# Optimization experiments

Hardware: AMD Instinct MI355X
Metric: run time of the kernel (lower is better)

Reference implementation:

```python
import jax, jax.numpy as jnp
import numpy as np

N = 50000
E = 800000
IN = 256
HID = 64
H12 = 4
LAT = 32
NEG_SLOPE = 0.2


def gat_conv(x, src, dst, W, a_src, a_dst, b, heads, out_ch, concat):
    """PyG GATConv (eval mode, add_self_loops already applied to src/dst).
    x: [N, F_in]; src/dst: [Etot]; W: [F_in, heads*out_ch]; a_*: [heads, out_ch]; b: bias.
    Returns (out, alpha[Etot, heads])."""
    n = x.shape[0]
    h = (x @ W).reshape(n, heads, out_ch)                 # [N,H,C]
    e_src = (h * a_src).sum(-1)                           # [N,H]
    e_dst = (h * a_dst).sum(-1)                           # [N,H]
    e = jax.nn.leaky_relu(e_src[src] + e_dst[dst], NEG_SLOPE)   # [Etot,H]
    emax = jax.ops.segment_max(e, dst, num_segments=n)
    ee = jnp.exp(e - emax[dst])
    denom = jax.ops.segment_sum(ee, dst, num_segments=n)
    alpha = ee / (denom[dst] + 1e-16)                     # segment softmax over incoming edges
    msg = h[src] * alpha[:, :, None]                      # [Etot,H,C]
    out = jax.ops.segment_sum(msg, dst, num_segments=n)   # [N,H,C]
    out = out.reshape(n, heads * out_ch) if concat else out.mean(axis=1)
    return out + b, alpha


def setup_inputs() -> dict:
    key = jax.random.key(0)
    ks = jax.random.split(key, 20)
    s = 0.1
    inp = {
        "x": jax.random.normal(ks[0], (N, IN), jnp.float32),
        "edge_index": jax.random.randint(ks[1], (2, E), 0, N, jnp.int32),
        "W1": jax.random.normal(ks[2], (IN, H12 * HID), jnp.float32) * s,
        "a1s": jax.random.normal(ks[3], (H12, HID), jnp.float32) * s,
        "a1d": jax.random.normal(ks[4], (H12, HID), jnp.float32) * s,
        "b1": jnp.zeros((H12 * HID,), jnp.float32),
        "W2": jax.random.normal(ks[5], (H12 * HID, H12 * HID), jnp.float32) * s,
        "a2s": jax.random.normal(ks[6], (H12, HID), jnp.float32) * s,
        "a2d": jax.random.normal(ks[7], (H12, HID), jnp.float32) * s,
        "b2": jnp.zeros((HID,), jnp.float32),
        "Wm": jax.random.normal(ks[8], (HID, LAT), jnp.float32) * s,
        "ams": jax.random.normal(ks[9], (1, LAT), jnp.float32) * s,
        "amd": jax.random.normal(ks[10], (1, LAT), jnp.float32) * s,
        "bm": jnp.zeros((LAT,), jnp.float32),
        # log_std head
        "Ws": jax.random.normal(ks[11], (HID, LAT), jnp.float32) * s,
        "ass": jax.random.normal(ks[12], (1, LAT), jnp.float32) * s,
        "asd": jax.random.normal(ks[13], (1, LAT), jnp.float32) * s,
        "bs": jnp.zeros((LAT,), jnp.float32),
    }
    return inp


def reference(x, edge_index, W1, a1s, a1d, b1, W2, a2s, a2d, b2,
              Wm, ams, amd, bm, Ws, ass, asd, bs):
    # GATConv adds self loops by default
    loops = jnp.arange(N, dtype=edge_index.dtype)
    src = jnp.concatenate([edge_index[0], loops])
    dst = jnp.concatenate([edge_index[1], loops])

    h1, a_w1 = gat_conv(x, src, dst, W1, a1s, a1d, b1, H12, HID, True)
    h1 = jax.nn.relu(h1)
    h2, a_w2 = gat_conv(h1, src, dst, W2, a2s, a2d, b2, H12, HID, False)
    h2 = jax.nn.relu(h2)  # dropout is identity in eval mode
    z_mean, a_wm = gat_conv(h2, src, dst, Wm, ams, amd, bm, 1, LAT, False)
    z_log_std, a_ws = gat_conv(h2, src, dst, Ws, ass, asd, bs, 1, LAT, False)
    return (z_mean, z_log_std, a_w1, a_w2, a_wm, a_ws)
```

## Files before the change

### kernel.cpp

```cpp
#include <hip/hip_runtime.h>
#include <cstdint>
#include <cstddef>

#define NN 50000
#define EE 800000
#define ETOT 850000
#define NEG_SLOPE 0.2f

typedef _Float16 f16;
typedef __attribute__((ext_vector_type(4))) _Float16 f16x4;
typedef __attribute__((ext_vector_type(8))) _Float16 f16x8;
typedef __attribute__((ext_vector_type(4))) float f32x4;


__global__ __launch_bounds__(256) void deg_kernel(const int* __restrict__ ei, int* __restrict__ deg) {
    int e = blockIdx.x * 256 + threadIdx.x;
    if (e >= ETOT) return;
    int d = (e < EE) ? ei[EE + e] : (e - EE);
    atomicAdd(&deg[d], 1);
}

__global__ __launch_bounds__(256) void scan1_kernel(const int* __restrict__ deg, int* __restrict__ offs,
                                                    int* __restrict__ bsum, int n) {
    __shared__ int sh[256];
    int i = blockIdx.x * 256 + threadIdx.x;
    int v = (i < n) ? deg[i] : 0;
    sh[threadIdx.x] = v;
    __syncthreads();
    for (int off = 1; off < 256; off <<= 1) {
        int t = (threadIdx.x >= off) ? sh[threadIdx.x - off] : 0;
        __syncthreads();
        sh[threadIdx.x] += t;
        __syncthreads();
    }
    if (i < n) offs[i] = sh[threadIdx.x] - v;
    if (threadIdx.x == 255) bsum[blockIdx.x] = sh[255];
}

__global__ __launch_bounds__(256) void scan2_kernel(int* __restrict__ bsum, int nb) {
    __shared__ int sh[256];
    int v = (threadIdx.x < nb) ? bsum[threadIdx.x] : 0;
    sh[threadIdx.x] = v;
    __syncthreads();
    for (int off = 1; off < 256; off <<= 1) {
        int t = (threadIdx.x >= off) ? sh[threadIdx.x - off] : 0;
        __syncthreads();
        sh[threadIdx.x] += t;
        __syncthreads();
    }
    if (threadIdx.x < nb) bsum[threadIdx.x] = sh[threadIdx.x] - v;
}

__global__ __launch_bounds__(256) void scan3_kernel(const int* __restrict__ bsum, int* __restrict__ offs,
                                                    int* __restrict__ cursor, int n) {
    int i = blockIdx.x * 256 + threadIdx.x;
    if (i < n) {
        int o = offs[i] + bsum[blockIdx.x];
        offs[i] = o;
        cursor[i] = o;
    }
}

__global__ __launch_bounds__(256) void fill_kernel(const int* __restrict__ ei, int* __restrict__ cursor,
                                                   int* __restrict__ csrc, int* __restrict__ ceid) {
    int e = blockIdx.x * 256 + threadIdx.x;
    if (e >= ETOT) return;
    int d, s;
    if (e < EE) { s = ei[e]; d = ei[EE + e]; } else { s = e - EE; d = e - EE; }
    int p = atomicAdd(&cursor[d], 1);
    csrc[p] = s;
    ceid[p] = e;
}


template<int K, bool AF32>
__global__ __launch_bounds__(256) void mfma_gemm(const void* __restrict__ Ap, const f16* __restrict__ Bt,
                                                 f16* __restrict__ C, int M, int N) {
    int w = threadIdx.x >> 6, lane = threadIdx.x & 63;
    int m0 = blockIdx.y * 128 + w * 32;
    int n0 = blockIdx.x * 64;
    int r = lane & 15, kb = lane >> 4;
    int ar0 = m0 + r;       if (ar0 > M - 1) ar0 = M - 1;
    int ar1 = m0 + 16 + r;  if (ar1 > M - 1) ar1 = M - 1;
    f32x4 acc[2][4] = {};
    const float* Af = (const float*)Ap;
    const f16*   Ah = (const f16*)Ap;
    size_t a0off = (size_t)ar0 * K + kb * 8;
    size_t a1off = (size_t)ar1 * K + kb * 8;
    const f16* bbase = Bt + (size_t)(n0 + r) * K + kb * 8;
    for (int k0 = 0; k0 < K; k0 += 32) {
        f16x8 a0, a1;
        if constexpr (AF32) {
            float4 l0 = *(const float4*)(Af + a0off + k0);
            float4 h0 = *(const float4*)(Af + a0off + k0 + 4);
            float4 l1 = *(const float4*)(Af + a1off + k0);
            float4 h1 = *(const float4*)(Af + a1off + k0 + 4);
            a0[0]=(f16)l0.x; a0[1]=(f16)l0.y; a0[2]=(f16)l0.z; a0[3]=(f16)l0.w;
            a0[4]=(f16)h0.x; a0[5]=(f16)h0.y; a0[6]=(f16)h0.z; a0[7]=(f16)h0.w;
            a1[0]=(f16)l1.x; a1[1]=(f16)l1.y; a1[2]=(f16)l1.z; a1[3]=(f16)l1.w;
            a1[4]=(f16)h1.x; a1[5]=(f16)h1.y; a1[6]=(f16)h1.z; a1[7]=(f16)h1.w;
        } else {
            a0 = *(const f16x8*)(Ah + a0off + k0);
            a1 = *(const f16x8*)(Ah + a1off + k0);
        }
#pragma unroll
        for (int ni = 0; ni < 4; ++ni) {
            f16x8 b = *(const f16x8*)(bbase + (size_t)ni * 16 * K + k0);
            acc[0][ni] = __builtin_amdgcn_mfma_f32_16x16x32_f16(a0, b, acc[0][ni], 0, 0, 0);
            acc[1][ni] = __builtin_amdgcn_mfma_f32_16x16x32_f16(a1, b, acc[1][ni], 0, 0, 0);
        }
    }
#pragma unroll
    for (int mi = 0; mi < 2; ++mi) {
#pragma unroll
        for (int i = 0; i < 4; ++i) {
            int row = m0 + mi * 16 + kb * 4 + i;
            if (row < M) {
#pragma unroll
                for (int ni = 0; ni < 4; ++ni)
                    C[(size_t)row * N + n0 + ni * 16 + r] = (f16)acc[mi][ni][i];
            }
        }
    }
}


__global__ __launch_bounds__(256) void packw_kernel(const float* __restrict__ W1, const float* __restrict__ W2,
                                                    const float* __restrict__ Wm, const float* __restrict__ Ws,
                                                    const float* __restrict__ ams, const float* __restrict__ ass,
                                                    const float* __restrict__ amd, const float* __restrict__ asd,
                                                    f16* __restrict__ Wt1, f16* __restrict__ Wt2,
                                                    f16* __restrict__ Wtms,
                                                    float* __restrict__ aS, float* __restrict__ aD) {
    int i = blockIdx.x * 256 + threadIdx.x;
    if (i < 65536) {
        int n = i >> 8, k = i & 255;
        Wt1[(size_t)n * 256 + k] = (f16)W1[(size_t)k * 256 + n];
        Wt2[(size_t)n * 256 + k] = (f16)W2[(size_t)k * 256 + n];
    }
    if (i < 4096) {
        int c = i >> 6, k = i & 63;
        float v = (c < 32) ? Wm[k * 32 + c] : Ws[k * 32 + (c - 32)];
        Wtms[(size_t)c * 64 + k] = (f16)v;
    }
    if (i < 64) {
        aS[i] = (i < 32) ? ams[i] : ass[i - 32];
        aD[i] = (i < 32) ? amd[i] : asd[i - 32];
    }
}


__global__ __launch_bounds__(256) void scores4_kernel(const f16* __restrict__ H, const float* __restrict__ aS,
                                                      const float* __restrict__ aD, float* __restrict__ es,
                                                      float* __restrict__ ed) {
    int wave = threadIdx.x >> 6, lane = threadIdx.x & 63;
    int n = blockIdx.x * 4 + wave;
    if (n >= NN) return;
    f16x4 h = *(const f16x4*)(H + (size_t)n * 256 + lane * 4);
    float4 s4 = *(const float4*)(aS + lane * 4);
    float4 d4 = *(const float4*)(aD + lane * 4);
    float hx = (float)h[0], hy = (float)h[1], hz = (float)h[2], hw = (float)h[3];
    float ps = hx * s4.x + hy * s4.y + hz * s4.z + hw * s4.w;
    float pd = hx * d4.x + hy * d4.y + hz * d4.z + hw * d4.w;
    for (int off = 1; off < 16; off <<= 1) { ps += __shfl_xor(ps, off); pd += __shfl_xor(pd, off); }
    if ((lane & 15) == 0) {
        int hh = lane >> 4;
        es[n * 4 + hh] = ps;
        ed[n * 4 + hh] = pd;
    }
}

__global__ __launch_bounds__(256) void scores_ms_kernel(const f16* __restrict__ H, const float* __restrict__ aS,
                                                        const float* __restrict__ aD, float* __restrict__ es,
                                                        float* __restrict__ ed) {
    int wave = threadIdx.x >> 6, lane = threadIdx.x & 63;
    int n = blockIdx.x * 4 + wave;
    if (n >= NN) return;
    float h = (float)H[(size_t)n * 64 + lane];
    float ps = h * aS[lane];
    float pd = h * aD[lane];
    for (int off = 1; off < 32; off <<= 1) { ps += __shfl_xor(ps, off); pd += __shfl_xor(pd, off); }
    if ((lane & 31) == 0) {
        int g = lane >> 5;
        es[n * 2 + g] = ps;
        ed[n * 2 + g] = pd;
    }
}

__device__ __forceinline__ float leaky(float v) { return v > 0.f ? v : NEG_SLOPE * v; }


__global__ __launch_bounds__(256) void agg_concat_kernel(
    const f16* __restrict__ H, const float* __restrict__ es, const float* __restrict__ ed,
    const int* __restrict__ offs, const int* __restrict__ csrc, const int* __restrict__ ceid,
    const float* __restrict__ bias, f16* __restrict__ out, float* __restrict__ alpha_out) {
    int wave = threadIdx.x >> 6, lane = threadIdx.x & 63;
    int n = blockIdx.x * 4 + wave;
    if (n >= NN) return;
    int start = offs[n];
    int end = (n + 1 < NN) ? offs[n + 1] : ETOT;
    int deg = end - start;
    int h16 = lane >> 4, sub = lane & 15;
    float edh = ed[n * 4 + h16];
    float dsum = 0.f;
    for (int j = sub; j < deg; j += 16) {
        int s = csrc[start + j];
        dsum += __expf(leaky(es[s * 4 + h16] + edh));
    }
    for (int off = 1; off < 16; off <<= 1) dsum += __shfl_xor(dsum, off);
    float inv = 1.f / (dsum + 1e-16f);
    int half = lane >> 5;
    int l5 = lane & 31;
    int hh = l5 >> 3;
    int c8 = l5 * 8;
    float invh = __shfl(inv, hh << 4);
    float edhh = __shfl(edh, hh << 4);
    bool writer = ((l5 & 7) == 0);
    float accv[8] = {};
    int j = half;
    for (; j + 6 < deg; j += 8) {
        int p0 = start + j, p1 = start + j + 2, p2 = start + j + 4, p3 = start + j + 6;
        int s0 = csrc[p0], s1 = csrc[p1], s2 = csrc[p2], s3 = csrc[p3];
        float a0 = __expf(leaky(es[s0 * 4 + hh] + edhh)) * invh;
        float a1 = __expf(leaky(es[s1 * 4 + hh] + edhh)) * invh;
        float a2 = __expf(leaky(es[s2 * 4 + hh] + edhh)) * invh;
        float a3 = __expf(leaky(es[s3 * 4 + hh] + edhh)) * invh;
        if (writer) {
            alpha_out[(size_t)ceid[p0] * 4 + hh] = a0;
            alpha_out[(size_t)ceid[p1] * 4 + hh] = a1;
            alpha_out[(size_t)ceid[p2] * 4 + hh] = a2;
            alpha_out[(size_t)ceid[p3] * 4 + hh] = a3;
        }
        f16x8 v0 = *(const f16x8*)(H + (size_t)s0 * 256 + c8);
        f16x8 v1 = *(const f16x8*)(H + (size_t)s1 * 256 + c8);
        f16x8 v2 = *(const f16x8*)(H + (size_t)s2 * 256 + c8);
        f16x8 v3 = *(const f16x8*)(H + (size_t)s3 * 256 + c8);
#pragma unroll
        for (int k = 0; k < 8; ++k)
            accv[k] += a0 * (float)v0[k] + a1 * (float)v1[k] + a2 * (float)v2[k] + a3 * (float)v3[k];
    }
    for (; j < deg; j += 2) {
        int p0 = start + j;
        int s0 = csrc[p0];
        float a0 = __expf(leaky(es[s0 * 4 + hh] + edhh)) * invh;
        if (writer) alpha_out[(size_t)ceid[p0] * 4 + hh] = a0;
        f16x8 v0 = *(const f16x8*)(H + (size_t)s0 * 256 + c8);
#pragma unroll
        for (int k = 0; k < 8; ++k) accv[k] += a0 * (float)v0[k];
    }
#pragma unroll
    for (int k = 0; k < 8; ++k) accv[k] += __shfl_xor(accv[k], 32);
    if (lane < 32) {
        f16x8 r;
#pragma unroll
        for (int k = 0; k < 8; ++k) r[k] = (f16)fmaxf(accv[k] + bias[c8 + k], 0.f);
        *(f16x8*)(out + (size_t)n * 256 + c8) = r;
    }
}


__global__ __launch_bounds__(256) void agg_mean_kernel(
    const f16* __restrict__ H, const float* __restrict__ es, const float* __restrict__ ed,
    const int* __restrict__ offs, const int* __restrict__ csrc, const int* __restrict__ ceid,
    const float* __restrict__ bias, f16* __restrict__ out, float* __restrict__ alpha_out) {
    int wave = threadIdx.x >> 6, lane = threadIdx.x & 63;
    int n = blockIdx.x * 4 + wave;
    if (n >= NN) return;
    int start = offs[n];
    int end = (n + 1 < NN) ? offs[n + 1] : ETOT;
    int deg = end - start;
    int h16 = lane >> 4, sub = lane & 15;
    float edh = ed[n * 4 + h16];
    float dsum = 0.f;
    for (int j = sub; j < deg; j += 16) {
        int s = csrc[start + j];
        dsum += __expf(leaky(es[s * 4 + h16] + edh));
    }
    for (int off = 1; off < 16; off <<= 1) dsum += __shfl_xor(dsum, off);
    float inv = 1.f / (dsum + 1e-16f);
    int half = lane >> 5;
    int l5 = lane & 31;
    int hh = l5 >> 3;
    int c8 = l5 * 8;
    float invh = __shfl(inv, hh << 4);
    float edhh = __shfl(edh, hh << 4);
    bool writer = ((l5 & 7) == 0);
    float accv[8] = {};
    int j = half;
    for (; j + 6 < deg; j += 8) {
        int p0 = start + j, p1 = start + j + 2, p2 = start + j + 4, p3 = start + j + 6;
        int s0 = csrc[p0], s1 = csrc[p1], s2 = csrc[p2], s3 = csrc[p3];
        float a0 = __expf(leaky(es[s0 * 4 + hh] + edhh)) * invh;
        float a1 = __expf(leaky(es[s1 * 4 + hh] + edhh)) * invh;
        float a2 = __expf(leaky(es[s2 * 4 + hh] + edhh)) * invh;
        float a3 = __expf(leaky(es[s3 * 4 + hh] + edhh)) * invh;
        if (writer) {
            alpha_out[(size_t)ceid[p0] * 4 + hh] = a0;
            alpha_out[(size_t)ceid[p1] * 4 + hh] = a1;
            alpha_out[(size_t)ceid[p2] * 4 + hh] = a2;
            alpha_out[(size_t)ceid[p3] * 4 + hh] = a3;
        }
        f16x8 v0 = *(const f16x8*)(H + (size_t)s0 * 256 + c8);
        f16x8 v1 = *(const f16x8*)(H + (size_t)s1 * 256 + c8);
        f16x8 v2 = *(const f16x8*)(H + (size_t)s2 * 256 + c8);
        f16x8 v3 = *(const f16x8*)(H + (size_t)s3 * 256 + c8);
#pragma unroll
        for (int k = 0; k < 8; ++k)
            accv[k] += a0 * (float)v0[k] + a1 * (float)v1[k] + a2 * (float)v2[k] + a3 * (float)v3[k];
    }
    for (; j < deg; j += 2) {
        int p0 = start + j;
        int s0 = csrc[p0];
        float a0 = __expf(leaky(es[s0 * 4 + hh] + edhh)) * invh;
        if (writer) alpha_out[(size_t)ceid[p0] * 4 + hh] = a0;
        f16x8 v0 = *(const f16x8*)(H + (size_t)s0 * 256 + c8);
#pragma unroll
        for (int k = 0; k < 8; ++k) accv[k] += a0 * (float)v0[k];
    }
#pragma unroll
    for (int k = 0; k < 8; ++k) {
        accv[k] += __shfl_xor(accv[k], 8);
        accv[k] += __shfl_xor(accv[k], 16);
        accv[k] += __shfl_xor(accv[k], 32);
    }
    if (lane < 8) {
        f16x8 r;
#pragma unroll
        for (int k = 0; k < 8; ++k) r[k] = (f16)fmaxf(accv[k] * 0.25f + bias[lane * 8 + k], 0.f);
        *(f16x8*)(out + (size_t)n * 64 + lane * 8) = r;
    }
}


__global__ __launch_bounds__(256) void agg_ms_kernel(
    const f16* __restrict__ H, const float* __restrict__ es, const float* __restrict__ ed,
    const int* __restrict__ offs, const int* __restrict__ csrc, const int* __restrict__ ceid,
    const float* __restrict__ bm, const float* __restrict__ bs,
    float* __restrict__ zmean, float* __restrict__ zlog,
    float* __restrict__ a_wm, float* __restrict__ a_ws) {
    int wave = threadIdx.x >> 6, lane = threadIdx.x & 63;
    int n = blockIdx.x * 4 + wave;
    if (n >= NN) return;
    int start = offs[n];
    int end = (n + 1 < NN) ? offs[n + 1] : ETOT;
    int deg = end - start;
    int g = lane >> 5, sub = lane & 31;
    float edg = ed[n * 2 + g];
    float dsum = 0.f;
    for (int j = sub; j < deg; j += 32) {
        int s = csrc[start + j];
        dsum += __expf(leaky(es[s * 2 + g] + edg));
    }
    for (int off = 1; off < 32; off <<= 1) dsum += __shfl_xor(dsum, off);
    float inv = 1.f / (dsum + 1e-16f);
    int slot = lane >> 3;
    int le = lane & 7;
    int g2 = le >> 2;
    int c8 = le * 8;
    float invg = __shfl(inv, g2 << 5);
    float edg2 = __shfl(edg, g2 << 5);
    float accv[8] = {};
    for (int j = slot; j < deg; j += 8) {
        int p = start + j;
        int s = csrc[p];
        float a = __expf(leaky(es[s * 2 + g2] + edg2)) * invg;
        if (le == 0) a_wm[ceid[p]] = a;
        else if (le == 4) a_ws[ceid[p]] = a;
        f16x8 v = *(const f16x8*)(H + (size_t)s * 64 + c8);
#pragma unroll
        for (int k = 0; k < 8; ++k) accv[k] += a * (float)v[k];
    }
#pragma unroll
    for (int k = 0; k < 8; ++k) {
        accv[k] += __shfl_xor(accv[k], 8);
        accv[k] += __shfl_xor(accv[k], 16);
        accv[k] += __shfl_xor(accv[k], 32);
    }
    if (lane < 4) {
        float4 r0, r1;
        int cb = lane * 8;
        r0.x = accv[0] + bm[cb + 0]; r0.y = accv[1] + bm[cb + 1];
        r0.z = accv[2] + bm[cb + 2]; r0.w = accv[3] + bm[cb + 3];
        r1.x = accv[4] + bm[cb + 4]; r1.y = accv[5] + bm[cb + 5];
        r1.z = accv[6] + bm[cb + 6]; r1.w = accv[7] + bm[cb + 7];
        *(float4*)(zmean + (size_t)n * 32 + cb) = r0;
        *(float4*)(zmean + (size_t)n * 32 + cb + 4) = r1;
    } else if (lane < 8) {
        float4 r0, r1;
        int cb = (lane - 4) * 8;
        r0.x = accv[0] + bs[cb + 0]; r0.y = accv[1] + bs[cb + 1];
        r0.z = accv[2] + bs[cb + 2]; r0.w = accv[3] + bs[cb + 3];
        r1.x = accv[4] + bs[cb + 4]; r1.y = accv[5] + bs[cb + 5];
        r1.z = accv[6] + bs[cb + 6]; r1.w = accv[7] + bs[cb + 7];
        *(float4*)(zlog + (size_t)n * 32 + cb) = r0;
        *(float4*)(zlog + (size_t)n * 32 + cb + 4) = r1;
    }
}


extern "C" void kernel_launch(void* const* d_in, const int* in_sizes, int n_in,
                              void* d_out, int out_size, void* d_ws, size_t ws_size,
                              hipStream_t stream) {
    const float* x   = (const float*)d_in[0];
    const int*   ei  = (const int*)d_in[1];
    const float* W1  = (const float*)d_in[2];
    const float* a1s = (const float*)d_in[3];
    const float* a1d = (const float*)d_in[4];
    const float* b1  = (const float*)d_in[5];
    const float* W2  = (const float*)d_in[6];
    const float* a2s = (const float*)d_in[7];
    const float* a2d = (const float*)d_in[8];
    const float* b2  = (const float*)d_in[9];
    const float* Wm  = (const float*)d_in[10];
    const float* ams = (const float*)d_in[11];
    const float* amd = (const float*)d_in[12];
    const float* bm  = (const float*)d_in[13];
    const float* Ws  = (const float*)d_in[14];
    const float* ass = (const float*)d_in[15];
    const float* asd = (const float*)d_in[16];
    const float* bs  = (const float*)d_in[17];

    float* out = (float*)d_out;
    float* zmean = out;
    float* zlog  = out + 1600000;
    float* a_w1  = out + 3200000;
    float* a_w2  = out + 6600000;
    float* a_wm  = out + 10000000;
    float* a_ws_o = out + 10850000;

    float* ws = (float*)d_ws;
    size_t o = 0;
    f16*   Hh   = (f16*)(ws + o); o += (size_t)NN * 128;
    f16*   h1h  = (f16*)(ws + o); o += (size_t)NN * 128;
    f16*   h2h  = (f16*)(ws + o); o += (size_t)NN * 32;
    float* es1  = ws + o; o += NN * 4;
    float* ed1  = ws + o; o += NN * 4;
    float* es2  = ws + o; o += NN * 4;
    float* ed2  = ws + o; o += NN * 4;
    float* esms = ws + o; o += NN * 2;
    float* edms = ws + o; o += NN * 2;
    f16*   Wt1  = (f16*)(ws + o); o += 32768;
    f16*   Wt2  = (f16*)(ws + o); o += 32768;
    f16*   Wtms = (f16*)(ws + o); o += 2048;
    float* aSms = ws + o; o += 64;
    float* aDms = ws + o; o += 64;
    int* deg    = (int*)(ws + o); o += NN;
    int* offs   = (int*)(ws + o); o += NN;
    int* cursor = (int*)(ws + o); o += NN;
    int* csrc   = (int*)(ws + o); o += ETOT;
    int* ceid   = (int*)(ws + o); o += ETOT;

    const int edgeBlocks = (ETOT + 255) / 256;
    const int nodeBlocks = (NN + 255) / 256;
    const int waveBlocks = (NN + 3) / 4;

    hipMemsetAsync(deg, 0, NN * sizeof(int), stream);
    deg_kernel<<<edgeBlocks, 256, 0, stream>>>(ei, deg);
    scan1_kernel<<<nodeBlocks, 256, 0, stream>>>(deg, offs, cursor , NN);
    scan2_kernel<<<1, 256, 0, stream>>>(cursor, nodeBlocks);
    scan3_kernel<<<nodeBlocks, 256, 0, stream>>>(cursor, offs, deg , NN);
    fill_kernel<<<edgeBlocks, 256, 0, stream>>>(ei, deg, csrc, ceid);

    packw_kernel<<<256, 256, 0, stream>>>(W1, W2, Wm, Ws, ams, ass, amd, asd, Wt1, Wt2, Wtms, aSms, aDms);

    dim3 gg1(4, (NN + 127) / 128);
    dim3 gg3(1, (NN + 127) / 128);
    mfma_gemm<256, true><<<gg1, 256, 0, stream>>>(x, Wt1, Hh, NN, 256);
    scores4_kernel<<<waveBlocks, 256, 0, stream>>>(Hh, a1s, a1d, es1, ed1);
    agg_concat_kernel<<<waveBlocks, 256, 0, stream>>>(Hh, es1, ed1, offs, csrc, ceid, b1, h1h, a_w1);

    mfma_gemm<256, false><<<gg1, 256, 0, stream>>>(h1h, Wt2, Hh, NN, 256);
    scores4_kernel<<<waveBlocks, 256, 0, stream>>>(Hh, a2s, a2d, es2, ed2);
    agg_mean_kernel<<<waveBlocks, 256, 0, stream>>>(Hh, es2, ed2, offs, csrc, ceid, b2, h2h, a_w2);

    mfma_gemm<64, false><<<gg3, 256, 0, stream>>>(h2h, Wtms, Hh, NN, 64);
    scores_ms_kernel<<<waveBlocks, 256, 0, stream>>>(Hh, aSms, aDms, esms, edms);
    agg_ms_kernel<<<waveBlocks, 256, 0, stream>>>(Hh, esms, edms, offs, csrc, ceid, bm, bs,
                                                  zmean, zlog, a_wm, a_ws_o);
}
```

Before: 546.6 us.

## Move attention-weight output to coalesced per-edge kernels and drop edge-id permutation

The aggregation kernels no longer scatter alpha values through the CSR edge-id array. Instead they store the per-node softmax inverse denominators, and new edge-parallel kernels recompute alpha in original edge order with coalesced vector stores. This removes the ceid array along with its fill-time writes and gather reads, at the cost of extra launches that re-read edge_index, the scores and the inverses. Aggregation blocks also shrink from four waves to two.

```diff
diff --git a/kernel.cpp b/kernel.cpp
--- a/kernel.cpp
+++ b/kernel.cpp
@@ -62,14 +62,13 @@
 }
 
 __global__ __launch_bounds__(256) void fill_kernel(const int* __restrict__ ei, int* __restrict__ cursor,
-                                                   int* __restrict__ csrc, int* __restrict__ ceid) {
+                                                   int* __restrict__ csrc) {
     int e = blockIdx.x * 256 + threadIdx.x;
     if (e >= ETOT) return;
     int d, s;
     if (e < EE) { s = ei[e]; d = ei[EE + e]; } else { s = e - EE; d = e - EE; }
     int p = atomicAdd(&cursor[d], 1);
     csrc[p] = s;
-    ceid[p] = e;
 }
 
 
@@ -190,12 +189,45 @@
 __device__ __forceinline__ float leaky(float v) { return v > 0.f ? v : NEG_SLOPE * v; }
 
 
-__global__ __launch_bounds__(256) void agg_concat_kernel(
+__global__ __launch_bounds__(256) void alpha4_kernel(const int* __restrict__ ei, const float* __restrict__ es,
+                                                     const float* __restrict__ ed, const float* __restrict__ inv,
+                                                     float* __restrict__ out4) {
+    int e = blockIdx.x * 256 + threadIdx.x;
+    if (e >= ETOT) return;
+    int s, d;
+    if (e < EE) { s = ei[e]; d = ei[EE + e]; } else { s = e - EE; d = e - EE; }
+    float4 esv = *(const float4*)(es + (size_t)s * 4);
+    float4 edv = *(const float4*)(ed + (size_t)d * 4);
+    float4 iv  = *(const float4*)(inv + (size_t)d * 4);
+    float4 r;
+    r.x = __expf(leaky(esv.x + edv.x)) * iv.x;
+    r.y = __expf(leaky(esv.y + edv.y)) * iv.y;
+    r.z = __expf(leaky(esv.z + edv.z)) * iv.z;
+    r.w = __expf(leaky(esv.w + edv.w)) * iv.w;
+    *(float4*)(out4 + (size_t)e * 4) = r;
+}
+
+__global__ __launch_bounds__(256) void alpha_ms_kernel(const int* __restrict__ ei, const float* __restrict__ es,
+                                                       const float* __restrict__ ed, const float* __restrict__ inv,
+                                                       float* __restrict__ awm, float* __restrict__ aws) {
+    int e = blockIdx.x * 256 + threadIdx.x;
+    if (e >= ETOT) return;
+    int s, d;
+    if (e < EE) { s = ei[e]; d = ei[EE + e]; } else { s = e - EE; d = e - EE; }
+    float2 esv = *(const float2*)(es + (size_t)s * 2);
+    float2 edv = *(const float2*)(ed + (size_t)d * 2);
+    float2 iv  = *(const float2*)(inv + (size_t)d * 2);
+    awm[e] = __expf(leaky(esv.x + edv.x)) * iv.x;
+    aws[e] = __expf(leaky(esv.y + edv.y)) * iv.y;
+}
+
+
+__global__ __launch_bounds__(128) void agg_concat_kernel(
     const f16* __restrict__ H, const float* __restrict__ es, const float* __restrict__ ed,
-    const int* __restrict__ offs, const int* __restrict__ csrc, const int* __restrict__ ceid,
-    const float* __restrict__ bias, f16* __restrict__ out, float* __restrict__ alpha_out) {
+    const int* __restrict__ offs, const int* __restrict__ csrc,
+    const float* __restrict__ bias, f16* __restrict__ out, float* __restrict__ invout) {
     int wave = threadIdx.x >> 6, lane = threadIdx.x & 63;
-    int n = blockIdx.x * 4 + wave;
+    int n = blockIdx.x * 2 + wave;
     if (n >= NN) return;
     int start = offs[n];
     int end = (n + 1 < NN) ? offs[n + 1] : ETOT;
@@ -209,13 +241,13 @@
     }
     for (int off = 1; off < 16; off <<= 1) dsum += __shfl_xor(dsum, off);
     float inv = 1.f / (dsum + 1e-16f);
+    if (sub == 0) invout[n * 4 + h16] = inv;
     int half = lane >> 5;
     int l5 = lane & 31;
     int hh = l5 >> 3;
     int c8 = l5 * 8;
     float invh = __shfl(inv, hh << 4);
     float edhh = __shfl(edh, hh << 4);
-    bool writer = ((l5 & 7) == 0);
     float accv[8] = {};
     int j = half;
     for (; j + 6 < deg; j += 8) {
@@ -225,12 +257,6 @@
         float a1 = __expf(leaky(es[s1 * 4 + hh] + edhh)) * invh;
         float a2 = __expf(leaky(es[s2 * 4 + hh] + edhh)) * invh;
         float a3 = __expf(leaky(es[s3 * 4 + hh] + edhh)) * invh;
-        if (writer) {
-            alpha_out[(size_t)ceid[p0] * 4 + hh] = a0;
-            alpha_out[(size_t)ceid[p1] * 4 + hh] = a1;
-            alpha_out[(size_t)ceid[p2] * 4 + hh] = a2;
-            alpha_out[(size_t)ceid[p3] * 4 + hh] = a3;
-        }
         f16x8 v0 = *(const f16x8*)(H + (size_t)s0 * 256 + c8);
         f16x8 v1 = *(const f16x8*)(H + (size_t)s1 * 256 + c8);
         f16x8 v2 = *(const f16x8*)(H + (size_t)s2 * 256 + c8);
@@ -243,7 +269,6 @@
         int p0 = start + j;
         int s0 = csrc[p0];
         float a0 = __expf(leaky(es[s0 * 4 + hh] + edhh)) * invh;
-        if (writer) alpha_out[(size_t)ceid[p0] * 4 + hh] = a0;
         f16x8 v0 = *(const f16x8*)(H + (size_t)s0 * 256 + c8);
 #pragma unroll
         for (int k = 0; k < 8; ++k) accv[k] += a0 * (float)v0[k];
@@ -259,12 +284,12 @@
 }
 
 
-__global__ __launch_bounds__(256) void agg_mean_kernel(
+__global__ __launch_bounds__(128) void agg_mean_kernel(
     const f16* __restrict__ H, const float* __restrict__ es, const float* __restrict__ ed,
-    const int* __restrict__ offs, const int* __restrict__ csrc, const int* __restrict__ ceid,
-    const float* __restrict__ bias, f16* __restrict__ out, float* __restrict__ alpha_out) {
+    const int* __restrict__ offs, const int* __restrict__ csrc,
+    const float* __restrict__ bias, f16* __restrict__ out, float* __restrict__ invout) {
     int wave = threadIdx.x >> 6, lane = threadIdx.x & 63;
-    int n = blockIdx.x * 4 + wave;
+    int n = blockIdx.x * 2 + wave;
     if (n >= NN) return;
     int start = offs[n];
     int end = (n + 1 < NN) ? offs[n + 1] : ETOT;
@@ -278,13 +303,13 @@
     }
     for (int off = 1; off < 16; off <<= 1) dsum += __shfl_xor(dsum, off);
     float inv = 1.f / (dsum + 1e-16f);
+    if (sub == 0) invout[n * 4 + h16] = inv;
     int half = lane >> 5;
     int l5 = lane & 31;
     int hh = l5 >> 3;
     int c8 = l5 * 8;
     float invh = __shfl(inv, hh << 4);
     float edhh = __shfl(edh, hh << 4);
-    bool writer = ((l5 & 7) == 0);
     float accv[8] = {};
     int j = half;
     for (; j + 6 < deg; j += 8) {
@@ -294,12 +319,6 @@
         float a1 = __expf(leaky(es[s1 * 4 + hh] + edhh)) * invh;
         float a2 = __expf(leaky(es[s2 * 4 + hh] + edhh)) * invh;
         float a3 = __expf(leaky(es[s3 * 4 + hh] + edhh)) * invh;
-        if (writer) {
-            alpha_out[(size_t)ceid[p0] * 4 + hh] = a0;
-            alpha_out[(size_t)ceid[p1] * 4 + hh] = a1;
-            alpha_out[(size_t)ceid[p2] * 4 + hh] = a2;
-            alpha_out[(size_t)ceid[p3] * 4 + hh] = a3;
-        }
         f16x8 v0 = *(const f16x8*)(H + (size_t)s0 * 256 + c8);
         f16x8 v1 = *(const f16x8*)(H + (size_t)s1 * 256 + c8);
         f16x8 v2 = *(const f16x8*)(H + (size_t)s2 * 256 + c8);
@@ -312,7 +331,6 @@
         int p0 = start + j;
         int s0 = csrc[p0];
         float a0 = __expf(leaky(es[s0 * 4 + hh] + edhh)) * invh;
-        if (writer) alpha_out[(size_t)ceid[p0] * 4 + hh] = a0;
         f16x8 v0 = *(const f16x8*)(H + (size_t)s0 * 256 + c8);
 #pragma unroll
         for (int k = 0; k < 8; ++k) accv[k] += a0 * (float)v0[k];
@@ -332,14 +350,13 @@
 }
 
 
-__global__ __launch_bounds__(256) void agg_ms_kernel(
+__global__ __launch_bounds__(128) void agg_ms_kernel(
     const f16* __restrict__ H, const float* __restrict__ es, const float* __restrict__ ed,
-    const int* __restrict__ offs, const int* __restrict__ csrc, const int* __restrict__ ceid,
+    const int* __restrict__ offs, const int* __restrict__ csrc,
     const float* __restrict__ bm, const float* __restrict__ bs,
-    float* __restrict__ zmean, float* __restrict__ zlog,
-    float* __restrict__ a_wm, float* __restrict__ a_ws) {
+    float* __restrict__ zmean, float* __restrict__ zlog, float* __restrict__ invout) {
     int wave = threadIdx.x >> 6, lane = threadIdx.x & 63;
-    int n = blockIdx.x * 4 + wave;
+    int n = blockIdx.x * 2 + wave;
     if (n >= NN) return;
     int start = offs[n];
     int end = (n + 1 < NN) ? offs[n + 1] : ETOT;
@@ -353,6 +370,7 @@
     }
     for (int off = 1; off < 32; off <<= 1) dsum += __shfl_xor(dsum, off);
     float inv = 1.f / (dsum + 1e-16f);
+    if (sub == 0) invout[n * 2 + g] = inv;
     int slot = lane >> 3;
     int le = lane & 7;
     int g2 = le >> 2;
@@ -364,8 +382,6 @@
         int p = start + j;
         int s = csrc[p];
         float a = __expf(leaky(es[s * 2 + g2] + edg2)) * invg;
-        if (le == 0) a_wm[ceid[p]] = a;
-        else if (le == 4) a_ws[ceid[p]] = a;
         f16x8 v = *(const f16x8*)(H + (size_t)s * 64 + c8);
 #pragma unroll
         for (int k = 0; k < 8; ++k) accv[k] += a * (float)v[k];
@@ -439,6 +455,9 @@
     float* ed2  = ws + o; o += NN * 4;
     float* esms = ws + o; o += NN * 2;
     float* edms = ws + o; o += NN * 2;
+    float* inv1 = ws + o; o += NN * 4;
+    float* inv2 = ws + o; o += NN * 4;
+    float* invms= ws + o; o += NN * 2;
     f16*   Wt1  = (f16*)(ws + o); o += 32768;
     f16*   Wt2  = (f16*)(ws + o); o += 32768;
     f16*   Wtms = (f16*)(ws + o); o += 2048;
@@ -448,18 +467,18 @@
     int* offs   = (int*)(ws + o); o += NN;
     int* cursor = (int*)(ws + o); o += NN;
     int* csrc   = (int*)(ws + o); o += ETOT;
-    int* ceid   = (int*)(ws + o); o += ETOT;
 
     const int edgeBlocks = (ETOT + 255) / 256;
     const int nodeBlocks = (NN + 255) / 256;
     const int waveBlocks = (NN + 3) / 4;
+    const int aggBlocks  = (NN + 1) / 2;
 
     hipMemsetAsync(deg, 0, NN * sizeof(int), stream);
     deg_kernel<<<edgeBlocks, 256, 0, stream>>>(ei, deg);
     scan1_kernel<<<nodeBlocks, 256, 0, stream>>>(deg, offs, cursor , NN);
     scan2_kernel<<<1, 256, 0, stream>>>(cursor, nodeBlocks);
     scan3_kernel<<<nodeBlocks, 256, 0, stream>>>(cursor, offs, deg , NN);
-    fill_kernel<<<edgeBlocks, 256, 0, stream>>>(ei, deg, csrc, ceid);
+    fill_kernel<<<edgeBlocks, 256, 0, stream>>>(ei, deg, csrc);
 
     packw_kernel<<<256, 256, 0, stream>>>(W1, W2, Wm, Ws, ams, ass, amd, asd, Wt1, Wt2, Wtms, aSms, aDms);
 
@@ -467,14 +486,17 @@
     dim3 gg3(1, (NN + 127) / 128);
     mfma_gemm<256, true><<<gg1, 256, 0, stream>>>(x, Wt1, Hh, NN, 256);
     scores4_kernel<<<waveBlocks, 256, 0, stream>>>(Hh, a1s, a1d, es1, ed1);
-    agg_concat_kernel<<<waveBlocks, 256, 0, stream>>>(Hh, es1, ed1, offs, csrc, ceid, b1, h1h, a_w1);
+    agg_concat_kernel<<<aggBlocks, 128, 0, stream>>>(Hh, es1, ed1, offs, csrc, b1, h1h, inv1);
+    alpha4_kernel<<<edgeBlocks, 256, 0, stream>>>(ei, es1, ed1, inv1, a_w1);
 
     mfma_gemm<256, false><<<gg1, 256, 0, stream>>>(h1h, Wt2, Hh, NN, 256);
     scores4_kernel<<<waveBlocks, 256, 0, stream>>>(Hh, a2s, a2d, es2, ed2);
-    agg_mean_kernel<<<waveBlocks, 256, 0, stream>>>(Hh, es2, ed2, offs, csrc, ceid, b2, h2h, a_w2);
+    agg_mean_kernel<<<aggBlocks, 128, 0, stream>>>(Hh, es2, ed2, offs, csrc, b2, h2h, inv2);
+    alpha4_kernel<<<edgeBlocks, 256, 0, stream>>>(ei, es2, ed2, inv2, a_w2);
 
     mfma_gemm<64, false><<<gg3, 256, 0, stream>>>(h2h, Wtms, Hh, NN, 64);
     scores_ms_kernel<<<waveBlocks, 256, 0, stream>>>(Hh, aSms, aDms, esms, edms);
-    agg_ms_kernel<<<waveBlocks, 256, 0, stream>>>(Hh, esms, edms, offs, csrc, ceid, bm, bs,
-                                                  zmean, zlog, a_wm, a_ws_o);
-}
+    agg_ms_kernel<<<aggBlocks, 128, 0, stream>>>(Hh, esms, edms, offs, csrc, bm, bs,
+                                                 zmean, zlog, invms);
+    alpha_ms_kernel<<<edgeBlocks, 256, 0, stream>>>(ei, esms, edms, invms, a_wm, a_ws_o);
+}
```

After: 544.0 us. No clear change (-0.5%).
